# Kernel tuning notes

Measured on AMD Instinct MI355X. Metric: run time of the kernel, lower is better.

The kernel has to match this reference:

```python
import jax, jax.numpy as jnp
import numpy as np

N = 50000   # num_nodes
E = 1600000 # edges (avg degree 32)
D = 256     # in_feats
H = 256     # n_hidden


def setup_inputs() -> dict:
    key = jax.random.key(0)
    ks = jax.random.split(key, 9)
    s = 1.0 / np.sqrt(D)
    return {
        "input_nodes": jnp.arange(N, dtype=jnp.int32),
        "edge_src": jax.random.randint(ks[0], (E,), 0, N, dtype=jnp.int32),
        "edge_dst": jax.random.randint(ks[1], (E,), 0, N, dtype=jnp.int32),
        "emb": jax.random.normal(ks[2], (N, D), jnp.float32) * 0.02,
        "W_self0": jax.random.normal(ks[3], (D, H), jnp.float32) * s,
        "W_neigh0": jax.random.normal(ks[4], (D, H), jnp.float32) * s,
        "b0": jnp.zeros((H,), jnp.float32),
        "W_self1": jax.random.normal(ks[5], (H, H), jnp.float32) * s,
        "W_neigh1": jax.random.normal(ks[6], (H, H), jnp.float32) * s,
        "b1": jnp.zeros((H,), jnp.float32),
    }


def _sage_mean(h, src, dst, W_self, W_neigh, b, n):
    # gather neighbor features, mean-reduce by destination, then linear.
    msgs = h[src]                                                  # [E, d]
    ssum = jax.ops.segment_sum(msgs, dst, num_segments=n)          # [n, d]
    deg = jax.ops.segment_sum(jnp.ones(src.shape, h.dtype), dst, num_segments=n)
    h_neigh = ssum / jnp.maximum(deg, 1.0)[:, None]
    return h @ W_self + h_neigh @ W_neigh + b


def reference(input_nodes, edge_src, edge_dst, emb,
              W_self0, W_neigh0, b0, W_self1, W_neigh1, b1):
    h = emb[input_nodes]                                            # [N, D]
    h = _sage_mean(h, edge_src, edge_dst, W_self0, W_neigh0, b0, N)
    h = jax.nn.relu(h)  # dropout is identity at inference
    h = _sage_mean(h, edge_src, edge_dst, W_self1, W_neigh1, b1, N)
    h = h / jnp.linalg.norm(h)  # global Frobenius norm, as in torch.norm(h)
    return h
```

## Files before the change

kernel.cpp:

```cpp
#include <hip/hip_runtime.h>
#include <math.h>

#define NN 50000
#define NE 1600000
#define DF 256
#define NBUCK 391
#define CHS4 ((long long)NN * 64)
#define HALFN 25000

typedef unsigned short ushortT;
typedef __attribute__((ext_vector_type(8))) short short8;
typedef __attribute__((ext_vector_type(4))) float floatx4;
typedef __attribute__((ext_vector_type(4))) unsigned uintx4;

__device__ __forceinline__ unsigned bf16rne(float f) {
    unsigned u = __float_as_uint(f);
    return (u + 0x7fffu + ((u >> 16) & 1u)) >> 16;
}

#define ASYNC16(gptr, ldsptr) \
    __builtin_amdgcn_global_load_lds((const __attribute__((address_space(1))) unsigned*)(gptr), \
                                     (__attribute__((address_space(3))) unsigned*)(ldsptr), 16, 0, 0)


__global__ void k_zero(int* __restrict__ bcnt) {
    int i = blockIdx.x * 256 + threadIdx.x;
    if (i < NBUCK) bcnt[i] = 0;
}

__global__ __launch_bounds__(256)
void k_bhist(const int* __restrict__ dst, int* __restrict__ bcnt) {
    __shared__ int h[NBUCK];
    for (int i = threadIdx.x; i < NBUCK; i += 256) h[i] = 0;
    __syncthreads();
    int base = blockIdx.x * 4096;
#pragma unroll
    for (int i = 0; i < 16; ++i) {
        int e = base + i * 256 + threadIdx.x;
        if (e < NE) atomicAdd(&h[dst[e] >> 7], 1);
    }
    __syncthreads();
    for (int i = threadIdx.x; i < NBUCK; i += 256)
        if (h[i]) atomicAdd(&bcnt[i], h[i]);
}

__global__ void k_bscan(const int* __restrict__ bcnt, int* __restrict__ bbase,
                        int* __restrict__ cursor, int* __restrict__ row_ptr,
                        float* __restrict__ nrm) {
    __shared__ int s[512];
    int t = threadIdx.x;
    int v = (t < NBUCK) ? bcnt[t] : 0;
    s[t] = v; __syncthreads();
    for (int off = 1; off < 512; off <<= 1) {
        int x = (t >= off) ? s[t - off] : 0;
        __syncthreads();
        s[t] += x;
        __syncthreads();
    }
    if (t < NBUCK) { bbase[t] = s[t] - v; cursor[t] = s[t] - v; }
    if (t == 0) { bbase[NBUCK] = NE; row_ptr[NN] = NE; *nrm = 0.0f; }
}

__global__ __launch_bounds__(256)
void k_bin(const int* __restrict__ src, const int* __restrict__ dst,
           int* __restrict__ cursor, unsigned* __restrict__ rec) {
    __shared__ int h[NBUCK];
    __shared__ int gb[NBUCK];
    for (int i = threadIdx.x; i < NBUCK; i += 256) h[i] = 0;
    __syncthreads();
    const int base = blockIdx.x * 2048;
    int bk[8], rk[8];
    unsigned pk[8];
#pragma unroll
    for (int i = 0; i < 8; ++i) {
        int e = base + i * 256 + threadIdx.x;
        if (e < NE) {
            int d = dst[e];
            bk[i] = d >> 7;
            pk[i] = (unsigned)src[e] | ((unsigned)(d & 127) << 16);
            rk[i] = atomicAdd(&h[bk[i]], 1);
        } else bk[i] = -1;
    }
    __syncthreads();
    for (int i = threadIdx.x; i < NBUCK; i += 256) {
        int c = h[i];
        gb[i] = c ? atomicAdd(&cursor[i], c) : 0;
    }
    __syncthreads();
#pragma unroll
    for (int i = 0; i < 8; ++i)
        if (bk[i] >= 0) rec[gb[bk[i]] + rk[i]] = pk[i];
}


__global__ __launch_bounds__(256)
void k_csr(const unsigned* __restrict__ rec, const int* __restrict__ bbase,
           int* __restrict__ row_ptr, int* __restrict__ hp, ushortT* __restrict__ csr) {
    __shared__ int cnt[256];
    __shared__ int cur[256];
    __shared__ int s[256];
    const int B = blockIdx.x, t = threadIdx.x;
    cnt[t] = 0;
    __syncthreads();
    const int beg = bbase[B], end = bbase[B + 1];
    for (int p = beg + t; p < end; p += 256) {
        unsigned r = rec[p];
        int idx = (int)((r >> 16) & 127) * 2 + ((r & 0xffffu) >= HALFN ? 1 : 0);
        atomicAdd(&cnt[idx], 1);
    }
    __syncthreads();
    int v = cnt[t];
    s[t] = v; __syncthreads();
    for (int off = 1; off < 256; off <<= 1) {
        int x = (t >= off) ? s[t - off] : 0;
        __syncthreads();
        s[t] += x;
        __syncthreads();
    }
    cur[t] = s[t] - v;
    __syncthreads();
    if (t < 128) {
        int node = B * 128 + t;
        if (node < NN) {
            row_ptr[node] = beg + s[2 * t] - cnt[2 * t];
            hp[node]      = beg + s[2 * t + 1] - cnt[2 * t + 1];
        }
    }
    for (int p = beg + t; p < end; p += 256) {
        unsigned r = rec[p];
        int idx = (int)((r >> 16) & 127) * 2 + ((r & 0xffffu) >= HALFN ? 1 : 0);
        int loc = atomicAdd(&cur[idx], 1);
        csr[beg + loc] = (ushortT)r;
    }
}


__global__ __launch_bounds__(256)
void k_cvt(const float* __restrict__ emb, const int* __restrict__ gather,
           ushortT* __restrict__ embb,
           const float* __restrict__ Ws0, const float* __restrict__ Wn0,
           ushortT* __restrict__ Wt0,
           const float* __restrict__ Ws1, const float* __restrict__ Wn1,
           ushortT* __restrict__ Wt1) {
    const int b = blockIdx.x;
    if (b < 6250) {
        long long i = ((long long)b * 256 + threadIdx.x) * 8;
        int row = (int)(i >> 8);
        int col = (int)(i & 255);
        long long g = (long long)gather[row] * 256 + col;
        float4 v0 = *(const float4*)(emb + g);
        float4 v1 = *(const float4*)(emb + g + 4);
        uint4 o;
        o.x = bf16rne(v0.x) | (bf16rne(v0.y) << 16);
        o.y = bf16rne(v0.z) | (bf16rne(v0.w) << 16);
        o.z = bf16rne(v1.x) | (bf16rne(v1.y) << 16);
        o.w = bf16rne(v1.z) | (bf16rne(v1.w) << 16);
        *(uint4*)(embb + ((long long)(col >> 6) * NN + row) * 64 + (col & 63)) = o;
    } else {
        const bool first = b < 6762;
        const int idx = ((first ? b - 6250 : b - 6762)) * 256 + threadIdx.x;
        const int n = idx >> 9;
        const int k = idx & 511;
        const float* Ws = first ? Ws0 : Ws1;
        const float* Wn = first ? Wn0 : Wn1;
        float v = (k < 256) ? Ws[k * 256 + n] : Wn[(k - 256) * 256 + n];
        (first ? Wt0 : Wt1)[idx] = (ushortT)bf16rne(v);
    }
}


__global__ __launch_bounds__(256)
void k_agg(const ushortT* __restrict__ feat, const int* __restrict__ row_ptr,
           const ushortT* __restrict__ csr, ushortT* __restrict__ out) {
    const int c    = blockIdx.x & 3;
    const int ng   = blockIdx.x >> 2;
    const int node = ng * 32 + (threadIdx.x >> 3);
    const int part = (threadIdx.x & 7) * 8;
    if (node >= NN) return;

    const ushortT* fc = feat + (long long)c * CHS4;
    const int beg = row_ptr[node], end = row_ptr[node + 1];

    float s[8] = {0.f, 0.f, 0.f, 0.f, 0.f, 0.f, 0.f, 0.f};

#define ACCUM(q) do { \
        s[0] += __uint_as_float(q.x << 16); \
        s[1] += __uint_as_float(q.x & 0xffff0000u); \
        s[2] += __uint_as_float(q.y << 16); \
        s[3] += __uint_as_float(q.y & 0xffff0000u); \
        s[4] += __uint_as_float(q.z << 16); \
        s[5] += __uint_as_float(q.z & 0xffff0000u); \
        s[6] += __uint_as_float(q.w << 16); \
        s[7] += __uint_as_float(q.w & 0xffff0000u); \
    } while (0)

    int p = beg;

    if (p < end && (p & 1)) {
        int i0 = (int)__builtin_nontemporal_load(csr + p);
        uintx4 q = *(const uintx4*)(fc + i0 * 64 + part);
        ACCUM(q);
        ++p;
    }

    unsigned x0 = 0, x1 = 0, x2 = 0, x3 = 0;
    if (p + 7 < end) {
        const unsigned* cp = (const unsigned*)(csr + p);
        x0 = __builtin_nontemporal_load(cp + 0);
        x1 = __builtin_nontemporal_load(cp + 1);
        x2 = __builtin_nontemporal_load(cp + 2);
        x3 = __builtin_nontemporal_load(cp + 3);
    }

    while (p + 7 < end) {
        uintx4 q0 = *(const uintx4*)(fc + (int)(x0 & 0xffffu) * 64 + part);
        uintx4 q1 = *(const uintx4*)(fc + (int)(x0 >> 16)     * 64 + part);
        uintx4 q2 = *(const uintx4*)(fc + (int)(x1 & 0xffffu) * 64 + part);
        uintx4 q3 = *(const uintx4*)(fc + (int)(x1 >> 16)     * 64 + part);
        uintx4 q4 = *(const uintx4*)(fc + (int)(x2 & 0xffffu) * 64 + part);
        uintx4 q5 = *(const uintx4*)(fc + (int)(x2 >> 16)     * 64 + part);
        uintx4 q6 = *(const uintx4*)(fc + (int)(x3 & 0xffffu) * 64 + part);
        uintx4 q7 = *(const uintx4*)(fc + (int)(x3 >> 16)     * 64 + part);

        const int np = p + 8;
        if (np + 7 < end) {
            const unsigned* cp = (const unsigned*)(csr + np);
            x0 = __builtin_nontemporal_load(cp + 0);
            x1 = __builtin_nontemporal_load(cp + 1);
            x2 = __builtin_nontemporal_load(cp + 2);
            x3 = __builtin_nontemporal_load(cp + 3);
        }

        ACCUM(q0); ACCUM(q1); ACCUM(q2); ACCUM(q3);
        ACCUM(q4); ACCUM(q5); ACCUM(q6); ACCUM(q7);
        p = np;
    }

    for (; p < end; ++p) {
        int i0 = (int)__builtin_nontemporal_load(csr + p);
        uintx4 q = *(const uintx4*)(fc + i0 * 64 + part);
        ACCUM(q);
    }
#undef ACCUM

    float inv = 1.0f / fmaxf((float)(end - beg), 1.0f);
    uintx4 o;
    o.x = bf16rne(s[0] * inv) | (bf16rne(s[1] * inv) << 16);
    o.y = bf16rne(s[2] * inv) | (bf16rne(s[3] * inv) << 16);
    o.z = bf16rne(s[4] * inv) | (bf16rne(s[5] * inv) << 16);
    o.w = bf16rne(s[6] * inv) | (bf16rne(s[7] * inv) << 16);
    __builtin_nontemporal_store(o, (uintx4*)(out + ((long long)c * NN + node) * 64 + part));
}


template<int RELU, int NORM>
__global__ __launch_bounds__(512, 2)
void k_gemm(const ushortT* __restrict__ Aself, const ushortT* __restrict__ Aneigh,
            const ushortT* __restrict__ Wt, const float* __restrict__ bias,
            ushortT* __restrict__ Cb, float* __restrict__ Cf, float* __restrict__ norm_acc) {
    __shared__ ushortT As[4096];
    __shared__ ushortT Bs[8192];
    __shared__ float red[8];

    const int t = threadIdx.x;
    const int w = t >> 6;
    const int lane = t & 63;
    const int wm = w >> 2;
    const int wn = w & 3;
    const int m0 = blockIdx.x * 128;

    const int ar = t >> 2;
    const int cu = (t & 3) * 8;

    const long long gA = (long long)min(m0 + ar, NN - 1) * 64 + cu;

    const unsigned ldsA = w * 512;
    const unsigned ldsB = w * 512;

    const int fm = lane & 15;
    const int fk = (lane >> 4) * 8;

    floatx4 acc[4][4];
#pragma unroll
    for (int i = 0; i < 4; ++i)
#pragma unroll
        for (int j = 0; j < 4; ++j) acc[i][j] = (floatx4){0.f, 0.f, 0.f, 0.f};

    for (int kt = 0; kt < 512; kt += 32) {
        const int kc = (kt < 256) ? kt : kt - 256;
        const ushortT* Ab = ((kt < 256) ? Aself : Aneigh)
                          + (long long)(kc >> 6) * CHS4 + (kc & 32);

        __syncthreads();
        ASYNC16(Ab + gA, As + ldsA);
#pragma unroll
        for (int i = 0; i < 2; ++i)
            ASYNC16(Wt + (i * 128 + ar) * 512 + kt + cu, Bs + i * 4096 + ldsB);
        __syncthreads();

        short8 af[4], bf[4];
#pragma unroll
        for (int i = 0; i < 4; ++i)
            af[i] = *(const short8*)&As[(wm * 64 + i * 16 + fm) * 32 + fk];
#pragma unroll
        for (int j = 0; j < 4; ++j)
            bf[j] = *(const short8*)&Bs[(wn * 64 + j * 16 + fm) * 32 + fk];
#pragma unroll
        for (int i = 0; i < 4; ++i)
#pragma unroll
            for (int j = 0; j < 4; ++j)
                acc[i][j] = __builtin_amdgcn_mfma_f32_16x16x32_bf16(af[i], bf[j], acc[i][j], 0, 0, 0);
    }

    float bj[4];
#pragma unroll
    for (int j = 0; j < 4; ++j) bj[j] = bias[wn * 64 + j * 16 + fm];

    float sumsq = 0.0f;
#pragma unroll
    for (int i = 0; i < 4; ++i) {
#pragma unroll
        for (int r = 0; r < 4; ++r) {
            const int row = m0 + wm * 64 + i * 16 + (lane >> 4) * 4 + r;
            if (row < NN) {
#pragma unroll
                for (int j = 0; j < 4; ++j) {
                    const int col = wn * 64 + j * 16 + fm;
                    float v = acc[i][j][r] + bj[j];
                    if (RELU) v = fmaxf(v, 0.0f);
                    if (NORM) {
                        Cf[(long long)row * 256 + col] = v;
                        sumsq += v * v;
                    } else {
                        Cb[((long long)(col >> 6) * NN + row) * 64 + (col & 63)] = (ushortT)bf16rne(v);
                    }
                }
            }
        }
    }

    if (NORM) {
#pragma unroll
        for (int off = 32; off > 0; off >>= 1) sumsq += __shfl_down(sumsq, off);
        if (lane == 0) red[w] = sumsq;
        __syncthreads();
        if (t == 0) {
            float tot = 0.f;
#pragma unroll
            for (int i = 0; i < 8; ++i) tot += red[i];
            atomicAdd(norm_acc, tot);
        }
    }
}

__global__ void k_scale(float* __restrict__ out, const float* __restrict__ nrm) {
    const float s = 1.0f / sqrtf(*nrm);
    long long i = ((long long)blockIdx.x * 256 + threadIdx.x) * 4;
    float4 v = *(float4*)&out[i];
    v.x *= s; v.y *= s; v.z *= s; v.w *= s;
    *(float4*)&out[i] = v;
}


extern "C" void kernel_launch(void* const* d_in, const int* in_sizes, int n_in,
                              void* d_out, int out_size, void* d_ws, size_t ws_size,
                              hipStream_t stream) {
    const int*   input_nodes = (const int*)d_in[0];
    const int*   esrc = (const int*)d_in[1];
    const int*   edst = (const int*)d_in[2];
    const float* emb  = (const float*)d_in[3];
    const float* Ws0  = (const float*)d_in[4];
    const float* Wn0  = (const float*)d_in[5];
    const float* b0   = (const float*)d_in[6];
    const float* Ws1  = (const float*)d_in[7];
    const float* Wn1  = (const float*)d_in[8];
    const float* b1   = (const float*)d_in[9];
    float* out = (float*)d_out;

    char* base = (char*)d_ws;
    ushortT*  embb    = (ushortT*) (base);
    ushortT*  h1b     = (ushortT*) (base + 25600000);
    ushortT*  hnb     = (ushortT*) (base + 51200000);
    unsigned* rec     = (unsigned*)(base + 76800000);
    ushortT*  csr     = (ushortT*) (base + 83200000);
    ushortT*  Wt0     = (ushortT*) (base + 86400000);
    ushortT*  Wt1     = (ushortT*) (base + 86662144);
    int*      row_ptr = (int*)     (base + 86924288);
    int*      hp      = (int*)     (base + 87124304);
    int*      bcnt    = (int*)     (base + 87324304);
    int*      bbase   = (int*)     (base + 87325904);
    int*      cursor  = (int*)     (base + 87327504);
    float*    nrm     = (float*)   (base + 87329104);

    k_zero  <<<2,     256, 0, stream>>>(bcnt);
    k_bhist <<<391,   256, 0, stream>>>(edst, bcnt);
    k_bscan <<<1,     512, 0, stream>>>(bcnt, bbase, cursor, row_ptr, nrm);
    k_bin   <<<782,   256, 0, stream>>>(esrc, edst, cursor, rec);
    k_csr   <<<NBUCK, 256, 0, stream>>>(rec, bbase, row_ptr, hp, csr);

    k_cvt<<<7274, 256, 0, stream>>>(emb, input_nodes, embb, Ws0, Wn0, Wt0, Ws1, Wn1, Wt1);

    const int GEMM_BLOCKS = (NN + 127) / 128;
    const int AGG_BLOCKS  = ((NN + 31) / 32) * 4;

    k_agg<<<AGG_BLOCKS, 256, 0, stream>>>(embb, row_ptr, csr, hnb);
    k_gemm<1, 0><<<GEMM_BLOCKS, 512, 0, stream>>>(embb, hnb, Wt0, b0, h1b, nullptr, nullptr);

    k_agg<<<AGG_BLOCKS, 256, 0, stream>>>(h1b, row_ptr, csr, hnb);
    k_gemm<0, 1><<<GEMM_BLOCKS, 512, 0, stream>>>(h1b, hnb, Wt1, b1, nullptr, out, nrm);

    k_scale<<<NN * DF / 4 / 256, 256, 0, stream>>>(out, nrm);
}
```

Baseline: 437.7 us.

## Make aggregation persistent over node passes, ordering neighbor reads by source half

The aggregation kernel now launches a fixed grid of 1024 blocks, and each thread handles seven nodes strided across the graph instead of one. It uses the per-node split point hp, which divides each CSR row into low-index and high-index sources. All seven nodes' first-half neighbors are accumulated first, then all second halves, so the whole grid works on one half of the feature table at a time to improve L2/MALL hit rates. The cost is seven sets of 8 accumulators per thread, which raises register pressure, plus less load balancing across blocks.

```diff
diff --git a/kernel.cpp b/kernel.cpp
--- a/kernel.cpp
+++ b/kernel.cpp
@@ -7,6 +7,9 @@
 #define NBUCK 391
 #define CHS4 ((long long)NN * 64)
 #define HALFN 25000
+#define PASSES 7
+#define AGSETS 256
+#define AGG_BLOCKS (AGSETS * 4)
 
 typedef unsigned short ushortT;
 typedef __attribute__((ext_vector_type(8))) short short8;
@@ -169,87 +172,103 @@
 }
 
 
-__global__ __launch_bounds__(256)
+#define ACCUM8(S, q) do { \
+        S[0] += __uint_as_float(q.x << 16); \
+        S[1] += __uint_as_float(q.x & 0xffff0000u); \
+        S[2] += __uint_as_float(q.y << 16); \
+        S[3] += __uint_as_float(q.y & 0xffff0000u); \
+        S[4] += __uint_as_float(q.z << 16); \
+        S[5] += __uint_as_float(q.z & 0xffff0000u); \
+        S[6] += __uint_as_float(q.w << 16); \
+        S[7] += __uint_as_float(q.w & 0xffff0000u); \
+    } while (0)
+
+#define ACC_RANGE(LO, HI, S) do { \
+        int p_ = (LO); const int hi_ = (HI); \
+        if (p_ < hi_ && (p_ & 1)) { \
+            int i0_ = (int)__builtin_nontemporal_load(csr + p_); \
+            uintx4 q_ = *(const uintx4*)(fc + i0_ * 64 + part); \
+            ACCUM8(S, q_); ++p_; \
+        } \
+        unsigned x0_ = 0, x1_ = 0, x2_ = 0, x3_ = 0; \
+        if (p_ + 7 < hi_) { \
+            const unsigned* cp_ = (const unsigned*)(csr + p_); \
+            x0_ = __builtin_nontemporal_load(cp_ + 0); \
+            x1_ = __builtin_nontemporal_load(cp_ + 1); \
+            x2_ = __builtin_nontemporal_load(cp_ + 2); \
+            x3_ = __builtin_nontemporal_load(cp_ + 3); \
+        } \
+        while (p_ + 7 < hi_) { \
+            uintx4 q0_ = *(const uintx4*)(fc + (int)(x0_ & 0xffffu) * 64 + part); \
+            uintx4 q1_ = *(const uintx4*)(fc + (int)(x0_ >> 16)     * 64 + part); \
+            uintx4 q2_ = *(const uintx4*)(fc + (int)(x1_ & 0xffffu) * 64 + part); \
+            uintx4 q3_ = *(const uintx4*)(fc + (int)(x1_ >> 16)     * 64 + part); \
+            uintx4 q4_ = *(const uintx4*)(fc + (int)(x2_ & 0xffffu) * 64 + part); \
+            uintx4 q5_ = *(const uintx4*)(fc + (int)(x2_ >> 16)     * 64 + part); \
+            uintx4 q6_ = *(const uintx4*)(fc + (int)(x3_ & 0xffffu) * 64 + part); \
+            uintx4 q7_ = *(const uintx4*)(fc + (int)(x3_ >> 16)     * 64 + part); \
+            const int np_ = p_ + 8; \
+            if (np_ + 7 < hi_) { \
+                const unsigned* cp_ = (const unsigned*)(csr + np_); \
+                x0_ = __builtin_nontemporal_load(cp_ + 0); \
+                x1_ = __builtin_nontemporal_load(cp_ + 1); \
+                x2_ = __builtin_nontemporal_load(cp_ + 2); \
+                x3_ = __builtin_nontemporal_load(cp_ + 3); \
+            } \
+            ACCUM8(S, q0_); ACCUM8(S, q1_); ACCUM8(S, q2_); ACCUM8(S, q3_); \
+            ACCUM8(S, q4_); ACCUM8(S, q5_); ACCUM8(S, q6_); ACCUM8(S, q7_); \
+            p_ = np_; \
+        } \
+        for (; p_ < hi_; ++p_) { \
+            int i0_ = (int)__builtin_nontemporal_load(csr + p_); \
+            uintx4 q_ = *(const uintx4*)(fc + i0_ * 64 + part); \
+            ACCUM8(S, q_); \
+        } \
+    } while (0)
+
+__global__ __launch_bounds__(256, 4)
 void k_agg(const ushortT* __restrict__ feat, const int* __restrict__ row_ptr,
-           const ushortT* __restrict__ csr, ushortT* __restrict__ out) {
+           const int* __restrict__ hp, const ushortT* __restrict__ csr,
+           ushortT* __restrict__ out) {
     const int c    = blockIdx.x & 3;
-    const int ng   = blockIdx.x >> 2;
-    const int node = ng * 32 + (threadIdx.x >> 3);
+    const int gset = blockIdx.x >> 2;
+    const int oct  = threadIdx.x >> 3;
     const int part = (threadIdx.x & 7) * 8;
-    if (node >= NN) return;
-
     const ushortT* fc = feat + (long long)c * CHS4;
-    const int beg = row_ptr[node], end = row_ptr[node + 1];
-
-    float s[8] = {0.f, 0.f, 0.f, 0.f, 0.f, 0.f, 0.f, 0.f};
-
-#define ACCUM(q) do { \
-        s[0] += __uint_as_float(q.x << 16); \
-        s[1] += __uint_as_float(q.x & 0xffff0000u); \
-        s[2] += __uint_as_float(q.y << 16); \
-        s[3] += __uint_as_float(q.y & 0xffff0000u); \
-        s[4] += __uint_as_float(q.z << 16); \
-        s[5] += __uint_as_float(q.z & 0xffff0000u); \
-        s[6] += __uint_as_float(q.w << 16); \
-        s[7] += __uint_as_float(q.w & 0xffff0000u); \
-    } while (0)
-
-    int p = beg;
-
-    if (p < end && (p & 1)) {
-        int i0 = (int)__builtin_nontemporal_load(csr + p);
-        uintx4 q = *(const uintx4*)(fc + i0 * 64 + part);
-        ACCUM(q);
-        ++p;
-    }
-
-    unsigned x0 = 0, x1 = 0, x2 = 0, x3 = 0;
-    if (p + 7 < end) {
-        const unsigned* cp = (const unsigned*)(csr + p);
-        x0 = __builtin_nontemporal_load(cp + 0);
-        x1 = __builtin_nontemporal_load(cp + 1);
-        x2 = __builtin_nontemporal_load(cp + 2);
-        x3 = __builtin_nontemporal_load(cp + 3);
-    }
-
-    while (p + 7 < end) {
-        uintx4 q0 = *(const uintx4*)(fc + (int)(x0 & 0xffffu) * 64 + part);
-        uintx4 q1 = *(const uintx4*)(fc + (int)(x0 >> 16)     * 64 + part);
-        uintx4 q2 = *(const uintx4*)(fc + (int)(x1 & 0xffffu) * 64 + part);
-        uintx4 q3 = *(const uintx4*)(fc + (int)(x1 >> 16)     * 64 + part);
-        uintx4 q4 = *(const uintx4*)(fc + (int)(x2 & 0xffffu) * 64 + part);
-        uintx4 q5 = *(const uintx4*)(fc + (int)(x2 >> 16)     * 64 + part);
-        uintx4 q6 = *(const uintx4*)(fc + (int)(x3 & 0xffffu) * 64 + part);
-        uintx4 q7 = *(const uintx4*)(fc + (int)(x3 >> 16)     * 64 + part);
-
-        const int np = p + 8;
-        if (np + 7 < end) {
-            const unsigned* cp = (const unsigned*)(csr + np);
-            x0 = __builtin_nontemporal_load(cp + 0);
-            x1 = __builtin_nontemporal_load(cp + 1);
-            x2 = __builtin_nontemporal_load(cp + 2);
-            x3 = __builtin_nontemporal_load(cp + 3);
+
+    int rbegv[PASSES], hbv[PASSES], rendv[PASSES];
+    float s[PASSES][8];
+
+#pragma unroll
+    for (int ps = 0; ps < PASSES; ++ps) {
+        const int node = (ps * AGSETS + gset) * 32 + oct;
+        if (node < NN) {
+            rbegv[ps] = row_ptr[node];
+            rendv[ps] = row_ptr[node + 1];
+            hbv[ps]   = hp[node];
+        } else { rbegv[ps] = 0; hbv[ps] = 0; rendv[ps] = 0; }
+#pragma unroll
+        for (int k = 0; k < 8; ++k) s[ps][k] = 0.f;
+    }
+
+#pragma unroll
+    for (int ps = 0; ps < PASSES; ++ps)
+        ACC_RANGE(rbegv[ps], hbv[ps], s[ps]);
+
+#pragma unroll
+    for (int ps = 0; ps < PASSES; ++ps) {
+        ACC_RANGE(hbv[ps], rendv[ps], s[ps]);
+        const int node = (ps * AGSETS + gset) * 32 + oct;
+        if (node < NN) {
+            const float inv = 1.0f / fmaxf((float)(rendv[ps] - rbegv[ps]), 1.0f);
+            uintx4 o;
+            o.x = bf16rne(s[ps][0] * inv) | (bf16rne(s[ps][1] * inv) << 16);
+            o.y = bf16rne(s[ps][2] * inv) | (bf16rne(s[ps][3] * inv) << 16);
+            o.z = bf16rne(s[ps][4] * inv) | (bf16rne(s[ps][5] * inv) << 16);
+            o.w = bf16rne(s[ps][6] * inv) | (bf16rne(s[ps][7] * inv) << 16);
+            __builtin_nontemporal_store(o, (uintx4*)(out + ((long long)c * NN + node) * 64 + part));
         }
-
-        ACCUM(q0); ACCUM(q1); ACCUM(q2); ACCUM(q3);
-        ACCUM(q4); ACCUM(q5); ACCUM(q6); ACCUM(q7);
-        p = np;
-    }
-
-    for (; p < end; ++p) {
-        int i0 = (int)__builtin_nontemporal_load(csr + p);
-        uintx4 q = *(const uintx4*)(fc + i0 * 64 + part);
-        ACCUM(q);
-    }
-#undef ACCUM
-
-    float inv = 1.0f / fmaxf((float)(end - beg), 1.0f);
-    uintx4 o;
-    o.x = bf16rne(s[0] * inv) | (bf16rne(s[1] * inv) << 16);
-    o.y = bf16rne(s[2] * inv) | (bf16rne(s[3] * inv) << 16);
-    o.z = bf16rne(s[4] * inv) | (bf16rne(s[5] * inv) << 16);
-    o.w = bf16rne(s[6] * inv) | (bf16rne(s[7] * inv) << 16);
-    __builtin_nontemporal_store(o, (uintx4*)(out + ((long long)c * NN + node) * 64 + part));
+    }
 }
 
 
@@ -401,12 +420,11 @@
     k_cvt<<<7274, 256, 0, stream>>>(emb, input_nodes, embb, Ws0, Wn0, Wt0, Ws1, Wn1, Wt1);
 
     const int GEMM_BLOCKS = (NN + 127) / 128;
-    const int AGG_BLOCKS  = ((NN + 31) / 32) * 4;
-
-    k_agg<<<AGG_BLOCKS, 256, 0, stream>>>(embb, row_ptr, csr, hnb);
+
+    k_agg<<<AGG_BLOCKS, 256, 0, stream>>>(embb, row_ptr, hp, csr, hnb);
     k_gemm<1, 0><<<GEMM_BLOCKS, 512, 0, stream>>>(embb, hnb, Wt0, b0, h1b, nullptr, nullptr);
 
-    k_agg<<<AGG_BLOCKS, 256, 0, stream>>>(h1b, row_ptr, csr, hnb);
+    k_agg<<<AGG_BLOCKS, 256, 0, stream>>>(h1b, row_ptr, hp, csr, hnb);
     k_gemm<0, 1><<<GEMM_BLOCKS, 512, 0, stream>>>(h1b, hnb, Wt1, b1, nullptr, out, nrm);
 
     k_scale<<<NN * DF / 4 / 256, 256, 0, stream>>>(out, nrm);
```

After: 535.1 us. +22.2%, slower.

## Stage GEMM epilogue through LDS for coalesced vector stores

Applied to the files above, without the earlier changes.

Restructures the GEMM epilogue so each wave writes its accumulator fragments into a shared LDS tile, after which the whole block writes contiguous 16-byte rows to global memory. The fp32 output path now computes the sum of squares during the coalesced store. This replaces scattered 2-byte and 4-byte per-lane stores with wide coalesced stores, at the cost of extra barriers and LDS traffic. It also raises the launch-bounds occupancy hint from 2 to 4 blocks and replaces the zeroing kernel with hipMemsetAsync.

```diff
diff --git a/kernel.cpp b/kernel.cpp
--- a/kernel.cpp
+++ b/kernel.cpp
@@ -22,11 +22,6 @@
     __builtin_amdgcn_global_load_lds((const __attribute__((address_space(1))) unsigned*)(gptr), \
                                      (__attribute__((address_space(3))) unsigned*)(ldsptr), 16, 0, 0)
 
-
-__global__ void k_zero(int* __restrict__ bcnt) {
-    int i = blockIdx.x * 256 + threadIdx.x;
-    if (i < NBUCK) bcnt[i] = 0;
-}
 
 __global__ __launch_bounds__(256)
 void k_bhist(const int* __restrict__ dst, int* __restrict__ bcnt) {
@@ -254,13 +249,14 @@
 
 
 template<int RELU, int NORM>
-__global__ __launch_bounds__(512, 2)
+__global__ __launch_bounds__(512, 4)
 void k_gemm(const ushortT* __restrict__ Aself, const ushortT* __restrict__ Aneigh,
             const ushortT* __restrict__ Wt, const float* __restrict__ bias,
             ushortT* __restrict__ Cb, float* __restrict__ Cf, float* __restrict__ norm_acc) {
-    __shared__ ushortT As[4096];
-    __shared__ ushortT Bs[8192];
+    __shared__ ushortT LDSBUF[12288];
     __shared__ float red[8];
+    ushortT* As = LDSBUF;
+    ushortT* Bs = LDSBUF + 4096;
 
     const int t = threadIdx.x;
     const int w = t >> 6;
@@ -316,30 +312,76 @@
 #pragma unroll
     for (int j = 0; j < 4; ++j) bj[j] = bias[wn * 64 + j * 16 + fm];
 
-    float sumsq = 0.0f;
-#pragma unroll
-    for (int i = 0; i < 4; ++i) {
-#pragma unroll
-        for (int r = 0; r < 4; ++r) {
-            const int row = m0 + wm * 64 + i * 16 + (lane >> 4) * 4 + r;
-            if (row < NN) {
-#pragma unroll
-                for (int j = 0; j < 4; ++j) {
-                    const int col = wn * 64 + j * 16 + fm;
-                    float v = acc[i][j][r] + bj[j];
-                    if (RELU) v = fmaxf(v, 0.0f);
-                    if (NORM) {
-                        Cf[(long long)row * 256 + col] = v;
-                        sumsq += v * v;
-                    } else {
-                        Cb[((long long)(col >> 6) * NN + row) * 64 + (col & 63)] = (ushortT)bf16rne(v);
+    __syncthreads();
+
+    if (!NORM) {
+        ushortT (*Cs)[256] = (ushortT(*)[256])LDSBUF;
+#pragma unroll
+        for (int g = 0; g < 4; ++g) {
+            if (wm == (g >> 1)) {
+#pragma unroll
+                for (int ii = 0; ii < 2; ++ii) {
+                    const int i = (g & 1) * 2 + ii;
+#pragma unroll
+                    for (int r = 0; r < 4; ++r) {
+                        const int lrow = ii * 16 + (lane >> 4) * 4 + r;
+#pragma unroll
+                        for (int j = 0; j < 4; ++j) {
+                            const int col = wn * 64 + j * 16 + fm;
+                            float v = acc[i][j][r] + bj[j];
+                            if (RELU) v = fmaxf(v, 0.0f);
+                            Cs[lrow][col] = (ushortT)bf16rne(v);
+                        }
                     }
                 }
             }
+            __syncthreads();
+#pragma unroll
+            for (int siter = 0; siter < 2; ++siter) {
+                const int id = t + siter * 512;
+                const int k8 = id & 7;
+                const int cc = (id >> 3) & 3;
+                const int lr = id >> 5;
+                const int R = m0 + g * 32 + lr;
+                if (R < NN) {
+                    uintx4 val = *(const uintx4*)&Cs[lr][cc * 64 + k8 * 8];
+                    *(uintx4*)(Cb + ((long long)cc * NN + R) * 64 + k8 * 8) = val;
+                }
+            }
+            __syncthreads();
         }
-    }
-
-    if (NORM) {
+    } else {
+        float (*Csf)[256] = (float(*)[256])LDSBUF;
+        float sumsq = 0.0f;
+#pragma unroll
+        for (int g = 0; g < 8; ++g) {
+            if (wm == (g >> 2)) {
+                const int i = g & 3;
+#pragma unroll
+                for (int r = 0; r < 4; ++r) {
+                    const int lrow = (lane >> 4) * 4 + r;
+#pragma unroll
+                    for (int j = 0; j < 4; ++j) {
+                        const int col = wn * 64 + j * 16 + fm;
+                        Csf[lrow][col] = acc[i][j][r] + bj[j];
+                    }
+                }
+            }
+            __syncthreads();
+#pragma unroll
+            for (int siter = 0; siter < 2; ++siter) {
+                const int id = t + siter * 512;
+                const int lr = id >> 6;
+                const int k  = id & 63;
+                const int R = m0 + g * 16 + lr;
+                if (R < NN) {
+                    float4 val = *(const float4*)&Csf[lr][k * 4];
+                    sumsq += val.x * val.x + val.y * val.y + val.z * val.z + val.w * val.w;
+                    *(float4*)(Cf + (long long)R * 256 + k * 4) = val;
+                }
+            }
+            __syncthreads();
+        }
 #pragma unroll
         for (int off = 32; off > 0; off >>= 1) sumsq += __shfl_down(sumsq, off);
         if (lane == 0) red[w] = sumsq;
@@ -392,7 +434,7 @@
     int*      cursor  = (int*)     (base + 87327504);
     float*    nrm     = (float*)   (base + 87329104);
 
-    k_zero  <<<2,     256, 0, stream>>>(bcnt);
+    hipMemsetAsync(bcnt, 0, NBUCK * sizeof(int), stream);
     k_bhist <<<391,   256, 0, stream>>>(edst, bcnt);
     k_bscan <<<1,     512, 0, stream>>>(bcnt, bbase, cursor, row_ptr, nrm);
     k_bin   <<<782,   256, 0, stream>>>(esrc, edst, cursor, rec);
```

Result: no change. 437.0 us (-0.2%).
